# Kernel optimization log

Hardware: AMD Instinct MI355X
Metric: run time of the kernel (lower is better)

## Reference

```python
import jax, jax.numpy as jnp
import numpy as np

L, H, HD, D, FF, V, S_LEN = 12, 12, 64, 768, 3072, 50257, 1024
NEG = jnp.finfo(jnp.float32).min


def _ln(x, g, b, eps=1e-5):
    mu = x.mean(-1, keepdims=True)
    var = ((x - mu) ** 2).mean(-1, keepdims=True)
    return (x - mu) * jax.lax.rsqrt(var + eps) * g + b


def setup_inputs() -> dict:
    key = jax.random.key(0)
    ks = jax.random.split(key, 14)
    n = lambda k, shp, s=0.02: jax.random.normal(k, shp, jnp.float32) * s
    return {
        "input_ids": jax.random.randint(ks[0], (1, S_LEN), 0, V, dtype=jnp.int32),
        "attention_mask": jnp.ones((1, S_LEN), jnp.int32),
        "wte": n(ks[1], (V, D)),
        "wpe": n(ks[2], (S_LEN, D)),
        "ln1_g": 1.0 + n(ks[3], (L, D), 0.01),
        "ln1_b": n(ks[4], (L, D), 0.01),
        "W_qkv": n(ks[5], (L, D, 3 * D)),
        "b_qkv": n(ks[6], (L, 3 * D)),
        "W_o": n(ks[7], (L, D, D)),
        "b_o": n(ks[8], (L, D)),
        "ln2_g": 1.0 + n(ks[9], (L, D), 0.01),
        "ln2_b": n(ks[10], (L, D), 0.01),
        "W_fc": n(ks[11], (L, D, FF)),
        "b_fc": n(ks[12], (L, FF)),
        "W_proj": n(ks[13], (L, FF, D)),
        "b_proj": jnp.zeros((L, D), jnp.float32),
        "S": 20, "Sa1": 21, "S2": 600,
    }


def reference(input_ids, attention_mask, wte, wpe, ln1_g, ln1_b, W_qkv, b_qkv,
              W_o, b_o, ln2_g, ln2_b, W_fc, b_fc, W_proj, b_proj, S, Sa1, S2):
    T = input_ids.shape[-1]
    h0 = wte[input_ids[0]] + wpe[:T]                      # [T, D]
    causal = jnp.tril(jnp.ones((T, T), bool))
    add_mask = (1.0 - attention_mask[0].astype(jnp.float32)) * NEG  # [T]
    scale = 1.0 / np.sqrt(HD).astype(np.float32)

    def step(h, p):
        (l1g, l1b, Wqkv, bqkv, Wo, bo, l2g, l2b, Wfc, bfc, Wp, bp) = p
        xl = _ln(h, l1g, l1b)                             # pre-block LN, [T, D]
        # ---- standard GPT-2 block forward (advances hidden state) ----
        qkv = xl @ Wqkv + bqkv
        q, k, v = jnp.split(qkv, 3, axis=-1)
        q = q.reshape(T, H, HD).transpose(1, 0, 2)        # [H, T, HD]
        k = k.reshape(T, H, HD).transpose(1, 0, 2)
        v = v.reshape(T, H, HD).transpose(1, 0, 2)
        sc = jnp.einsum('hqd,hkd->hqk', q, k) * scale
        sc = jnp.where(causal, sc, NEG) + add_mask
        ctx = jnp.einsum('hqk,hkd->hqd', jax.nn.softmax(sc, axis=-1), v)
        attn_out = ctx.transpose(1, 0, 2).reshape(T, D) @ Wo + bo
        h2 = h + attn_out
        h_new = h2 + (jax.nn.gelu(_ln(h2, l2g, l2b) @ Wfc + bfc,
                                  approximate=True) @ Wp + bp)
        # ---- manual QK circuit decomposition (pre-block hidden state) ----
        Wq, Wk, _ = jnp.split(Wqkv, 3, axis=1)            # [D, D] each
        bq, bk, _ = jnp.split(bqkv, 3, axis=0)            # [D] each
        Wmhq = Wq.reshape(D, H, HD).transpose(1, 0, 2)    # [H, D, HD]
        Wmhk = Wk.reshape(D, H, HD).transpose(1, 0, 2)
        bqh = bq.reshape(H, HD)                           # [H, HD]
        bkh = bk.reshape(H, HD)
        qc = jnp.einsum('td,hdk->htk', xl, Wmhq)          # x W_q per head
        kc = jnp.einsum('td,hdk->htk', xl, Wmhk)          # x W_k per head
        term1 = jnp.einsum('hqk,htk->hqt', qc, kc)                 # x Wq Wk^T x^T
        term2 = jnp.einsum('hk,htk->ht', bqh, kc)[:, None, :]      # bq Wk^T x^T
        term3 = jnp.einsum('hqk,hk->hq', qc, bkh)[:, :, None]      # x Wq bk^T
        term4 = jnp.einsum('hk,hk->h', bqh, bkh)[:, None, None]    # bq bk^T
        scores = (term1 + term2 + term3 + term4) * scale
        aw = jax.nn.softmax(jnp.where(causal, scores, NEG), axis=-1)  # [H, T, T]
        dup = aw[:, S2, S]
        ind = aw[:, S2, Sa1]
        prev = aw[:, -1, S2]
        return h_new, (dup, ind, prev, prev)

    params = (ln1_g, ln1_b, W_qkv, b_qkv, W_o, b_o,
              ln2_g, ln2_b, W_fc, b_fc, W_proj, b_proj)
    _, (dup, ind, prev, name) = jax.lax.scan(step, h0, params)
    return dup, ind, prev, name   # each [L, H] = [12, 12]
```

## Files before the change

kernel.cpp:

```cpp
#include <hip/hip_runtime.h>
#include <hip/hip_bf16.h>
#include <math.h>

namespace {

constexpr int T = 1024;
constexpr int D = 768;
constexpr int FF = 3072;
constexpr int H = 12;
constexpr int HD = 64;
constexpr int L = 12;
constexpr float SCALE = 0.125f;

typedef __attribute__((ext_vector_type(8))) short short8;
typedef __attribute__((ext_vector_type(4))) float floatx4;

__device__ inline unsigned short f2bf(float f) {
    __hip_bfloat16 h = __float2bfloat16(f);
    return *reinterpret_cast<unsigned short*>(&h);
}
__device__ inline float bf2f(unsigned short u) {
    union { unsigned int i; float f; } c;
    c.i = (unsigned int)u << 16;
    return c.f;
}
__device__ inline void gld16(const void* g, void* l) {
    __builtin_amdgcn_global_load_lds(
        (const __attribute__((address_space(1))) void*)g,
        (__attribute__((address_space(3))) void*)l, 16, 0, 0);
}

__global__ void embed_kernel(const int* __restrict__ ids,
                             const float* __restrict__ wte,
                             const float* __restrict__ wpe,
                             float* __restrict__ h) {
    int i = blockIdx.x * blockDim.x + threadIdx.x;
    if (i >= T * D) return;
    int t = i / D, d = i % D;
    h[i] = wte[(long)ids[t] * D + d] + wpe[i];
}

__global__ __launch_bounds__(256)
void ln_kernel(const float* __restrict__ x, const float* __restrict__ g,
               const float* __restrict__ b, unsigned short* __restrict__ out) {
    int row = blockIdx.x, tid = threadIdx.x;
    const float* xr = x + (long)row * D;
    float v0 = xr[tid], v1 = xr[tid + 256], v2 = xr[tid + 512];
    __shared__ float red[4];
    __shared__ float share;
    float s = v0 + v1 + v2;
#pragma unroll
    for (int o = 32; o; o >>= 1) s += __shfl_down(s, o, 64);
    if ((tid & 63) == 0) red[tid >> 6] = s;
    __syncthreads();
    if (tid == 0) share = (red[0] + red[1] + red[2] + red[3]) * (1.0f / D);
    __syncthreads();
    float mu = share;
    float d0 = v0 - mu, d1 = v1 - mu, d2 = v2 - mu;
    float q = d0 * d0 + d1 * d1 + d2 * d2;
#pragma unroll
    for (int o = 32; o; o >>= 1) q += __shfl_down(q, o, 64);
    __syncthreads();
    if ((tid & 63) == 0) red[tid >> 6] = q;
    __syncthreads();
    if (tid == 0) share = rsqrtf((red[0] + red[1] + red[2] + red[3]) * (1.0f / D) + 1e-5f);
    __syncthreads();
    float rs = share;
    unsigned short* orow = out + (long)row * D;
    orow[tid]       = f2bf(d0 * rs * g[tid]       + b[tid]);
    orow[tid + 256] = f2bf(d1 * rs * g[tid + 256] + b[tid + 256]);
    orow[tid + 512] = f2bf(d2 * rs * g[tid + 512] + b[tid + 512]);
}

__global__ __launch_bounds__(256)
void wconvert_b(const float* __restrict__ W, unsigned short* __restrict__ WT,
                int K, int N) {
    const int zl = blockIdx.z;
    W  += (long)zl * K * N;
    WT += (long)zl * N * K;
    __shared__ float t[32][33];
    const int n0 = blockIdx.x * 32, k0 = blockIdx.y * 32;
    const int tx = threadIdx.x, ty = threadIdx.y;
#pragma unroll
    for (int i = 0; i < 4; i++)
        t[ty * 4 + i][tx] = W[(long)(k0 + ty * 4 + i) * N + n0 + tx];
    __syncthreads();
#pragma unroll
    for (int i = 0; i < 4; i++)
        WT[(long)(n0 + ty * 4 + i) * K + k0 + tx] = f2bf(t[tx][ty * 4 + i]);
}

#define GEMM_CORE(KLEN)                                                                 \
    floatx4 acc[2][4] = {};                                                             \
    gld16(ApA, &As[0][ablk][0][0]);                                                     \
    gld16(ApB, &As[0][ablk + 4][0][0]);                                                 \
    gld16(Bp,  &Bs[0][ablk][0][0]);                                                     \
    __syncthreads();                                                                    \
    const int nsteps = (KLEN) >> 5;                                                     \
    for (int s = 0; s < nsteps; s++) {                                                  \
        const int buf = s & 1;                                                          \
        const int nb = buf ^ 1;                                                         \
        if (s + 1 < nsteps) {                                                           \
            gld16(ApA + (s + 1) * 32, &As[nb][ablk][0][0]);                             \
            gld16(ApB + (s + 1) * 32, &As[nb][ablk + 4][0][0]);                         \
            gld16(Bp  + (s + 1) * 32, &Bs[nb][ablk][0][0]);                             \
        }                                                                               \
        short8 af[2], bfr[4];                                                           \
        _Pragma("unroll")                                                               \
        for (int mi = 0; mi < 2; mi++)                                                  \
            af[mi] = *(const short8*)&As[buf][w * 2 + mi][lane][0];                     \
        _Pragma("unroll")                                                               \
        for (int ni = 0; ni < 4; ni++)                                                  \
            bfr[ni] = *(const short8*)&Bs[buf][ni][lane][0];                            \
        _Pragma("unroll")                                                               \
        for (int mi = 0; mi < 2; mi++)                                                  \
            _Pragma("unroll")                                                           \
            for (int ni = 0; ni < 4; ni++)                                              \
                acc[mi][ni] = __builtin_amdgcn_mfma_f32_16x16x32_bf16(                  \
                    af[mi], bfr[ni], acc[mi][ni], 0, 0, 0);                             \
        __syncthreads();                                                                \
    }

#define GEMM_PRELUDE(KOFF)                                                              \
    const int tid = threadIdx.x;                                                        \
    const int w = tid >> 6, lane = tid & 63;                                            \
    const int ablk = tid >> 6;                                                          \
    const int sl = tid & 63;                                                            \
    const int row0 = blockIdx.y * 128, col0 = blockIdx.x * 64;                          \
    __shared__ unsigned short As[2][8][64][8];                                          \
    __shared__ unsigned short Bs[2][4][64][8];                                          \
    const unsigned short* ApA = A + (long)(row0 + ablk * 16 + (sl & 15)) * K + (KOFF) + (sl >> 4) * 8; \
    const unsigned short* ApB = ApA + 64L * K;                                          \
    const unsigned short* Bp  = BT + (long)(col0 + ablk * 16 + (sl & 15)) * K + (KOFF) + (sl >> 4) * 8;

__global__ __launch_bounds__(256)
void gemm_fused(const unsigned short* __restrict__ A, const unsigned short* __restrict__ BT,
                const float* __restrict__ bias, unsigned short* __restrict__ Cb,
                int N, int K, int flags) {
    GEMM_PRELUDE(0)
    GEMM_CORE(K)
#pragma unroll
    for (int mi = 0; mi < 2; mi++) {
        int rg = row0 + (w * 2 + mi) * 16 + (lane >> 4) * 4;
#pragma unroll
        for (int ni = 0; ni < 4; ni++) {
            int cg = col0 + ni * 16 + (lane & 15);
            float bv = (flags & 1) ? bias[cg] : 0.f;
            float bscale = ((flags & 16) && cg < D) ? SCALE : 1.0f;
#pragma unroll
            for (int r = 0; r < 4; r++) {
                float v = acc[mi][ni][r] + bv;
                if (flags & 4) {
                    float zz = 0.7978845608028654f * (v + 0.044715f * v * v * v);
                    v = v / (1.0f + __expf(-2.0f * zz));
                }
                Cb[(long)(rg + r) * N + cg] = f2bf(v * bscale);
            }
        }
    }
}

__global__ __launch_bounds__(256)
void gemm_bf16(const unsigned short* __restrict__ A, const unsigned short* __restrict__ BT,
               float* __restrict__ part, int N, int K, int splitK) {
    const int z = blockIdx.z;
    const int Kc = K / splitK;
    GEMM_PRELUDE(z * Kc)
    GEMM_CORE(Kc)
    float* dst = part + (long)z * T * N;
#pragma unroll
    for (int mi = 0; mi < 2; mi++) {
        int rg = row0 + (w * 2 + mi) * 16 + (lane >> 4) * 4;
#pragma unroll
        for (int ni = 0; ni < 4; ni++) {
            int cg = col0 + ni * 16 + (lane & 15);
#pragma unroll
            for (int r = 0; r < 4; r++)
                dst[(long)(rg + r) * N + cg] = acc[mi][ni][r];
        }
    }
}

__global__ __launch_bounds__(256)
void reduce_ln(const float* __restrict__ part, const float* __restrict__ bias,
               const float* __restrict__ resid,
               const float* __restrict__ g, const float* __restrict__ b,
               float* __restrict__ Cres, unsigned short* __restrict__ Cln,
               int splitK) {
    const int row = blockIdx.x, tid = threadIdx.x;
    const int c0 = tid, c1 = tid + 256, c2 = tid + 512;
    const long rb = (long)row * D;
    float v0 = bias[c0] + resid[rb + c0];
    float v1 = bias[c1] + resid[rb + c1];
    float v2 = bias[c2] + resid[rb + c2];
    for (int z = 0; z < splitK; z++) {
        const float* p = part + (long)z * T * D + rb;
        v0 += p[c0]; v1 += p[c1]; v2 += p[c2];
    }
    float* crow = Cres + rb;
    crow[c0] = v0; crow[c1] = v1; crow[c2] = v2;
    __shared__ float red[4];
    __shared__ float share;
    float s = v0 + v1 + v2;
#pragma unroll
    for (int o = 32; o; o >>= 1) s += __shfl_down(s, o, 64);
    if ((tid & 63) == 0) red[tid >> 6] = s;
    __syncthreads();
    if (tid == 0) share = (red[0] + red[1] + red[2] + red[3]) * (1.0f / D);
    __syncthreads();
    float mu = share;
    float d0 = v0 - mu, d1 = v1 - mu, d2 = v2 - mu;
    float q = d0 * d0 + d1 * d1 + d2 * d2;
#pragma unroll
    for (int o = 32; o; o >>= 1) q += __shfl_down(q, o, 64);
    __syncthreads();
    if ((tid & 63) == 0) red[tid >> 6] = q;
    __syncthreads();
    if (tid == 0) share = rsqrtf((red[0] + red[1] + red[2] + red[3]) * (1.0f / D) + 1e-5f);
    __syncthreads();
    float rs = share;
    unsigned short* orow = Cln + rb;
    orow[c0] = f2bf(d0 * rs * g[c0] + b[c0]);
    orow[c1] = f2bf(d1 * rs * g[c1] + b[c1]);
    orow[c2] = f2bf(d2 * rs * g[c2] + b[c2]);
}

__device__ void probe_body(const unsigned short* __restrict__ qkvb,
                           const int* __restrict__ Sp, const int* __restrict__ Sa1p,
                           const int* __restrict__ S2p,
                           float* __restrict__ out, int layer, int which, int h) {
    const int s = *Sp, sa1 = *Sa1p, s2 = *S2p;
    const int row = which ? (T - 1) : s2;
    const int tid = threadIdx.x;
    __shared__ float qrow[64];
    __shared__ float prob[T];
    __shared__ float red[4];
    __shared__ float bshare;
    if (tid < 64) qrow[tid] = bf2f(qkvb[(long)row * (3 * D) + h * HD + tid]);
    __syncthreads();
    float mloc = -INFINITY;
    for (int j = tid; j <= row; j += 256) {
        const unsigned short* krow = qkvb + (long)j * (3 * D) + D + h * HD;
        float acc = 0;
#pragma unroll
        for (int d = 0; d < 64; d += 8) {
            short8 kv = *(const short8*)(krow + d);
#pragma unroll
            for (int e = 0; e < 8; e++)
                acc += qrow[d + e] * bf2f((unsigned short)kv[e]);
        }
        prob[j] = acc;
        mloc = fmaxf(mloc, acc);
    }
#pragma unroll
    for (int o = 32; o; o >>= 1) mloc = fmaxf(mloc, __shfl_down(mloc, o, 64));
    if ((tid & 63) == 0) red[tid >> 6] = mloc;
    __syncthreads();
    if (tid == 0) bshare = fmaxf(fmaxf(red[0], red[1]), fmaxf(red[2], red[3]));
    __syncthreads();
    float m = bshare;
    float ssum = 0;
    for (int j = tid; j <= row; j += 256) {
        float e = expf(prob[j] - m);
        prob[j] = e;
        ssum += e;
    }
#pragma unroll
    for (int o = 32; o; o >>= 1) ssum += __shfl_down(ssum, o, 64);
    __syncthreads();
    if ((tid & 63) == 0) red[tid >> 6] = ssum;
    __syncthreads();
    if (tid == 0) bshare = red[0] + red[1] + red[2] + red[3];
    __syncthreads();
    float inv = 1.0f / bshare;
    if (tid == 0) {
        if (which == 0) {
            out[0 * (L * H) + layer * H + h] = prob[s] * inv;
            out[1 * (L * H) + layer * H + h] = prob[sa1] * inv;
        } else {
            out[2 * (L * H) + layer * H + h] = prob[s2] * inv;
            out[3 * (L * H) + layer * H + h] = prob[s2] * inv;
        }
    }
}

__global__ __launch_bounds__(256)
void probe_kernel(const unsigned short* __restrict__ qkvb,
                  const int* __restrict__ Sp, const int* __restrict__ Sa1p,
                  const int* __restrict__ S2p,
                  float* __restrict__ out, int layer) {
    probe_body(qkvb, Sp, Sa1p, S2p, out, layer, blockIdx.x, blockIdx.y);
}

__global__ __launch_bounds__(256)
void flash_probe(const unsigned short* __restrict__ qkvb, unsigned short* __restrict__ ctxb,
                 const int* __restrict__ Sp, const int* __restrict__ Sa1p,
                 const int* __restrict__ S2p, float* __restrict__ out, int layer) {
    const int h = blockIdx.y;
    if (blockIdx.x >= T / 64) {
        probe_body(qkvb, Sp, Sa1p, S2p, out, layer, blockIdx.x - T / 64, h);
        return;
    }
    const int q0 = blockIdx.x * 64;
    const int tid = threadIdx.x;
    const int w = tid >> 6;
    const int l = tid & 63;
    const int lm = l & 15;
    const int g = l >> 4;

    __shared__ unsigned short Kl[64][72];
    __shared__ unsigned short Vt[64][80];
    __shared__ unsigned short Pl[4][16][72];

    short8 qf[2];
    {
        const unsigned short* qp = qkvb + (long)(q0 + w * 16 + lm) * (3 * D) + h * HD + g * 8;
        qf[0] = *(const short8*)(qp);
        qf[1] = *(const short8*)(qp + 32);
    }

    const int d8 = (tid & 7) * 8;
    const int kp = (tid >> 3) * 2;

    float m = -INFINITY, lsum = 0.f;
    floatx4 o[4] = {};
    const int qw = q0 + w * 16;
    const int nt = blockIdx.x + 1;

    for (int t = 0; t < nt; t++) {
        const int c0 = t * 64;
        __syncthreads();
        {
            const unsigned short* kr0 = qkvb + (long)(c0 + kp) * (3 * D) + D + h * HD + d8;
            const unsigned short* kr1 = kr0 + 3 * D;
            *(short8*)&Kl[kp][d8]     = *(const short8*)kr0;
            *(short8*)&Kl[kp + 1][d8] = *(const short8*)kr1;
            short8 va = *(const short8*)(kr0 + D);
            short8 vb = *(const short8*)(kr1 + D);
#pragma unroll
            for (int j = 0; j < 8; j++) {
                unsigned int pk = (unsigned)(unsigned short)va[j] |
                                  ((unsigned)(unsigned short)vb[j] << 16);
                *(unsigned int*)&Vt[d8 + j][kp] = pk;
            }
        }
        __syncthreads();

        if (c0 > qw + 15) continue;

        floatx4 st[4] = {};
#pragma unroll
        for (int ks = 0; ks < 2; ks++)
#pragma unroll
            for (int mt = 0; mt < 4; mt++) {
                short8 af = *(const short8*)&Kl[mt * 16 + lm][ks * 32 + g * 8];
                st[mt] = __builtin_amdgcn_mfma_f32_16x16x32_bf16(af, qf[ks], st[mt], 0, 0, 0);
            }

        const int qg = qw + lm;
        if (c0 + 63 > qw) {
#pragma unroll
            for (int mt = 0; mt < 4; mt++)
#pragma unroll
                for (int r = 0; r < 4; r++)
                    if (c0 + mt * 16 + g * 4 + r > qg) st[mt][r] = -INFINITY;
        }
        float tmax = -INFINITY;
#pragma unroll
        for (int mt = 0; mt < 4; mt++)
#pragma unroll
            for (int r = 0; r < 4; r++) tmax = fmaxf(tmax, st[mt][r]);
        tmax = fmaxf(tmax, __shfl_xor(tmax, 16));
        tmax = fmaxf(tmax, __shfl_xor(tmax, 32));
        float mn = fmaxf(m, tmax);
        float alpha = __expf(m - mn);
        float psum = 0.f;
        unsigned short pb[16];
#pragma unroll
        for (int mt = 0; mt < 4; mt++)
#pragma unroll
            for (int r = 0; r < 4; r++) {
                float p = __expf(st[mt][r] - mn);
                psum += p;
                pb[mt * 4 + r] = f2bf(p);
            }
        lsum = lsum * alpha + psum;
        m = mn;
#pragma unroll
        for (int mt = 0; mt < 4; mt++) {
            unsigned int p0 = (unsigned)pb[mt * 4 + 0] | ((unsigned)pb[mt * 4 + 1] << 16);
            unsigned int p1 = (unsigned)pb[mt * 4 + 2] | ((unsigned)pb[mt * 4 + 3] << 16);
            *(unsigned int*)&Pl[w][lm][mt * 16 + g * 4]     = p0;
            *(unsigned int*)&Pl[w][lm][mt * 16 + g * 4 + 2] = p1;
        }
        float ar0 = __shfl(alpha, g * 4 + 0), ar1 = __shfl(alpha, g * 4 + 1);
        float ar2 = __shfl(alpha, g * 4 + 2), ar3 = __shfl(alpha, g * 4 + 3);
#pragma unroll
        for (int fd = 0; fd < 4; fd++) {
            o[fd][0] *= ar0; o[fd][1] *= ar1; o[fd][2] *= ar2; o[fd][3] *= ar3;
        }
#pragma unroll
        for (int ks = 0; ks < 2; ks++) {
            short8 pa = *(const short8*)&Pl[w][lm][ks * 32 + g * 8];
#pragma unroll
            for (int fd = 0; fd < 4; fd++) {
                short8 vb = *(const short8*)&Vt[fd * 16 + lm][ks * 32 + g * 8];
                o[fd] = __builtin_amdgcn_mfma_f32_16x16x32_bf16(pa, vb, o[fd], 0, 0, 0);
            }
        }
    }
    float l2 = lsum + __shfl_xor(lsum, 16);
    float l4 = l2 + __shfl_xor(l2, 32);
    float linv = 1.0f / l4;
    float lr0 = __shfl(linv, g * 4 + 0), lr1 = __shfl(linv, g * 4 + 1);
    float lr2 = __shfl(linv, g * 4 + 2), lr3 = __shfl(linv, g * 4 + 3);
#pragma unroll
    for (int fd = 0; fd < 4; fd++) {
        unsigned short* cp = ctxb + (long)(qw + g * 4) * D + h * HD + fd * 16 + lm;
        cp[0 * D] = f2bf(o[fd][0] * lr0);
        cp[1 * D] = f2bf(o[fd][1] * lr1);
        cp[2 * D] = f2bf(o[fd][2] * lr2);
        cp[3 * D] = f2bf(o[fd][3] * lr3);
    }
}

}

extern "C" void kernel_launch(void* const* d_in, const int* in_sizes, int n_in,
                              void* d_out, int out_size, void* d_ws, size_t ws_size,
                              hipStream_t stream) {
    const int*   ids    = (const int*)  d_in[0];
    const float* wte    = (const float*)d_in[2];
    const float* wpe    = (const float*)d_in[3];
    const float* ln1_g  = (const float*)d_in[4];
    const float* ln1_b  = (const float*)d_in[5];
    const float* W_qkv  = (const float*)d_in[6];
    const float* b_qkv  = (const float*)d_in[7];
    const float* W_o    = (const float*)d_in[8];
    const float* b_o    = (const float*)d_in[9];
    const float* ln2_g  = (const float*)d_in[10];
    const float* ln2_b  = (const float*)d_in[11];
    const float* W_fc   = (const float*)d_in[12];
    const float* b_fc   = (const float*)d_in[13];
    const float* W_proj = (const float*)d_in[14];
    const float* b_proj = (const float*)d_in[15];
    const int*   Sp     = (const int*)  d_in[16];
    const int*   Sa1p   = (const int*)  d_in[17];
    const int*   S2p    = (const int*)  d_in[18];
    float* out = (float*)d_out;

    float* ws   = (float*)d_ws;
    float* h    = ws;
    float* h2   = h   + (long)T * D;
    float* part = h2  + (long)T * D;
    unsigned short* xl   = (unsigned short*)(part + 4L * T * D);
    unsigned short* qkvb = xl   + (long)T * D;
    unsigned short* ctxb = qkvb + (long)T * 3 * D;
    unsigned short* fb   = ctxb + (long)T * D;
    unsigned short* wt_qkv  = fb      + (long)T * FF;
    unsigned short* wt_o    = wt_qkv  + (long)L * 3 * D * D;
    unsigned short* wt_fc   = wt_o    + (long)L * D * D;
    unsigned short* wt_proj = wt_fc   + (long)L * D * FF;

    embed_kernel<<<(T * D + 255) / 256, 256, 0, stream>>>(ids, wte, wpe, h);
    wconvert_b<<<dim3(3 * D / 32, D / 32, L), dim3(32, 8), 0, stream>>>(W_qkv, wt_qkv, D, 3 * D);
    wconvert_b<<<dim3(D / 32, D / 32, L), dim3(32, 8), 0, stream>>>(W_o, wt_o, D, D);
    wconvert_b<<<dim3(FF / 32, D / 32, L), dim3(32, 8), 0, stream>>>(W_fc, wt_fc, D, FF);
    wconvert_b<<<dim3(D / 32, FF / 32, L), dim3(32, 8), 0, stream>>>(W_proj, wt_proj, FF, D);
    ln_kernel<<<T, 256, 0, stream>>>(h, ln1_g, ln1_b, xl);

    for (int l = 0; l < L; l++) {
        gemm_fused<<<dim3(3 * D / 64, T / 128), 256, 0, stream>>>(
            xl, wt_qkv + (long)l * 3 * D * D, b_qkv + (long)l * 3 * D,
            qkvb, 3 * D, D, 1 | 16);

        if (l == L - 1) {
            probe_kernel<<<dim3(2, H), 256, 0, stream>>>(qkvb, Sp, Sa1p, S2p, out, l);
            break;
        }

        flash_probe<<<dim3(T / 64 + 2, H), 256, 0, stream>>>(
            qkvb, ctxb, Sp, Sa1p, S2p, out, l);
        gemm_bf16<<<dim3(D / 64, T / 128, 4), 256, 0, stream>>>(
            ctxb, wt_o + (long)l * D * D, part, D, D, 4);
        reduce_ln<<<T, 256, 0, stream>>>(
            part, b_o + (long)l * D, h, ln2_g + l * D, ln2_b + l * D, h2, xl, 4);
        gemm_fused<<<dim3(FF / 64, T / 128), 256, 0, stream>>>(
            xl, wt_fc + (long)l * D * FF, b_fc + (long)l * FF, fb, FF, D, 1 | 4);
        gemm_bf16<<<dim3(D / 64, T / 128, 4), 256, 0, stream>>>(
            fb, wt_proj + (long)l * D * FF, part, D, FF, 4);
        reduce_ln<<<T, 256, 0, stream>>>(
            part, b_proj + (long)l * D, h2, ln1_g + (l + 1) * D, ln1_b + (l + 1) * D, h, xl, 4);
    }
}
```

Measured before the change: 1.357 ms.

## Split attention key tiles across wave pairs with 32-query blocks and merge

The flash attention kernel now processes 32 queries per block instead of 64, with two waves sharing each 16-query group. Each wave in a pair handles half of every 64-key tile, and the two partial softmax states are merged through shared memory at the end. The goal is to double the number of blocks and remove idle waves on the causal diagonal, improving occupancy and load balance. In exchange, each block loads K/V tiles for fewer queries, adds a cross-wave reduction, and uses a finite mask value instead of -inf.

```diff
diff --git a/kernel.cpp b/kernel.cpp
--- a/kernel.cpp
+++ b/kernel.cpp
@@ -11,6 +11,7 @@
 constexpr int HD = 64;
 constexpr int L = 12;
 constexpr float SCALE = 0.125f;
+constexpr float MNEG = -1.0e30f;
 
 typedef __attribute__((ext_vector_type(8))) short short8;
 typedef __attribute__((ext_vector_type(4))) float floatx4;
@@ -297,13 +298,15 @@
                  const int* __restrict__ Sp, const int* __restrict__ Sa1p,
                  const int* __restrict__ S2p, float* __restrict__ out, int layer) {
     const int h = blockIdx.y;
-    if (blockIdx.x >= T / 64) {
-        probe_body(qkvb, Sp, Sa1p, S2p, out, layer, blockIdx.x - T / 64, h);
+    if (blockIdx.x >= T / 32) {
+        probe_body(qkvb, Sp, Sa1p, S2p, out, layer, blockIdx.x - T / 32, h);
         return;
     }
-    const int q0 = blockIdx.x * 64;
+    const int q0 = blockIdx.x * 32;
     const int tid = threadIdx.x;
     const int w = tid >> 6;
+    const int pair = w >> 1;
+    const int sub = w & 1;
     const int l = tid & 63;
     const int lm = l & 15;
     const int g = l >> 4;
@@ -312,9 +315,11 @@
     __shared__ unsigned short Vt[64][80];
     __shared__ unsigned short Pl[4][16][72];
 
+    const int qw = q0 + pair * 16;
+
     short8 qf[2];
     {
-        const unsigned short* qp = qkvb + (long)(q0 + w * 16 + lm) * (3 * D) + h * HD + g * 8;
+        const unsigned short* qp = qkvb + (long)(qw + lm) * (3 * D) + h * HD + g * 8;
         qf[0] = *(const short8*)(qp);
         qf[1] = *(const short8*)(qp + 32);
     }
@@ -322,10 +327,9 @@
     const int d8 = (tid & 7) * 8;
     const int kp = (tid >> 3) * 2;
 
-    float m = -INFINITY, lsum = 0.f;
+    float m = MNEG, lsum = 0.f;
     floatx4 o[4] = {};
-    const int qw = q0 + w * 16;
-    const int nt = blockIdx.x + 1;
+    const int nt = blockIdx.x / 2 + 1;
 
     for (int t = 0; t < nt; t++) {
         const int c0 = t * 64;
@@ -346,52 +350,48 @@
         }
         __syncthreads();
 
-        if (c0 > qw + 15) continue;
-
-        floatx4 st[4] = {};
+        floatx4 st[2] = {};
 #pragma unroll
         for (int ks = 0; ks < 2; ks++)
 #pragma unroll
-            for (int mt = 0; mt < 4; mt++) {
-                short8 af = *(const short8*)&Kl[mt * 16 + lm][ks * 32 + g * 8];
-                st[mt] = __builtin_amdgcn_mfma_f32_16x16x32_bf16(af, qf[ks], st[mt], 0, 0, 0);
+            for (int m2 = 0; m2 < 2; m2++) {
+                short8 af = *(const short8*)&Kl[(sub * 2 + m2) * 16 + lm][ks * 32 + g * 8];
+                st[m2] = __builtin_amdgcn_mfma_f32_16x16x32_bf16(af, qf[ks], st[m2], 0, 0, 0);
             }
 
         const int qg = qw + lm;
-        if (c0 + 63 > qw) {
-#pragma unroll
-            for (int mt = 0; mt < 4; mt++)
+        const int cb = c0 + sub * 32;
+        if (cb + 31 > qw) {
+#pragma unroll
+            for (int m2 = 0; m2 < 2; m2++)
 #pragma unroll
                 for (int r = 0; r < 4; r++)
-                    if (c0 + mt * 16 + g * 4 + r > qg) st[mt][r] = -INFINITY;
-        }
-        float tmax = -INFINITY;
-#pragma unroll
-        for (int mt = 0; mt < 4; mt++)
-#pragma unroll
-            for (int r = 0; r < 4; r++) tmax = fmaxf(tmax, st[mt][r]);
+                    if (cb + m2 * 16 + g * 4 + r > qg) st[m2][r] = MNEG;
+        }
+        float tmax = fmaxf(fmaxf(fmaxf(st[0][0], st[0][1]), fmaxf(st[0][2], st[0][3])),
+                           fmaxf(fmaxf(st[1][0], st[1][1]), fmaxf(st[1][2], st[1][3])));
         tmax = fmaxf(tmax, __shfl_xor(tmax, 16));
         tmax = fmaxf(tmax, __shfl_xor(tmax, 32));
         float mn = fmaxf(m, tmax);
         float alpha = __expf(m - mn);
         float psum = 0.f;
-        unsigned short pb[16];
-#pragma unroll
-        for (int mt = 0; mt < 4; mt++)
+        unsigned short pb[8];
+#pragma unroll
+        for (int m2 = 0; m2 < 2; m2++)
 #pragma unroll
             for (int r = 0; r < 4; r++) {
-                float p = __expf(st[mt][r] - mn);
+                float p = __expf(st[m2][r] - mn);
                 psum += p;
-                pb[mt * 4 + r] = f2bf(p);
+                pb[m2 * 4 + r] = f2bf(p);
             }
         lsum = lsum * alpha + psum;
         m = mn;
 #pragma unroll
-        for (int mt = 0; mt < 4; mt++) {
-            unsigned int p0 = (unsigned)pb[mt * 4 + 0] | ((unsigned)pb[mt * 4 + 1] << 16);
-            unsigned int p1 = (unsigned)pb[mt * 4 + 2] | ((unsigned)pb[mt * 4 + 3] << 16);
-            *(unsigned int*)&Pl[w][lm][mt * 16 + g * 4]     = p0;
-            *(unsigned int*)&Pl[w][lm][mt * 16 + g * 4 + 2] = p1;
+        for (int m2 = 0; m2 < 2; m2++) {
+            unsigned int p0 = (unsigned)pb[m2 * 4 + 0] | ((unsigned)pb[m2 * 4 + 1] << 16);
+            unsigned int p1 = (unsigned)pb[m2 * 4 + 2] | ((unsigned)pb[m2 * 4 + 3] << 16);
+            *(unsigned int*)&Pl[w][lm][(sub * 2 + m2) * 16 + g * 4]     = p0;
+            *(unsigned int*)&Pl[w][lm][(sub * 2 + m2) * 16 + g * 4 + 2] = p1;
         }
         float ar0 = __shfl(alpha, g * 4 + 0), ar1 = __shfl(alpha, g * 4 + 1);
         float ar2 = __shfl(alpha, g * 4 + 2), ar3 = __shfl(alpha, g * 4 + 3);
@@ -399,28 +399,48 @@
         for (int fd = 0; fd < 4; fd++) {
             o[fd][0] *= ar0; o[fd][1] *= ar1; o[fd][2] *= ar2; o[fd][3] *= ar3;
         }
-#pragma unroll
-        for (int ks = 0; ks < 2; ks++) {
-            short8 pa = *(const short8*)&Pl[w][lm][ks * 32 + g * 8];
+        {
+            short8 pa = *(const short8*)&Pl[w][lm][sub * 32 + g * 8];
 #pragma unroll
             for (int fd = 0; fd < 4; fd++) {
-                short8 vb = *(const short8*)&Vt[fd * 16 + lm][ks * 32 + g * 8];
+                short8 vb = *(const short8*)&Vt[fd * 16 + lm][sub * 32 + g * 8];
                 o[fd] = __builtin_amdgcn_mfma_f32_16x16x32_bf16(pa, vb, o[fd], 0, 0, 0);
             }
         }
     }
     float l2 = lsum + __shfl_xor(lsum, 16);
     float l4 = l2 + __shfl_xor(l2, 32);
-    float linv = 1.0f / l4;
-    float lr0 = __shfl(linv, g * 4 + 0), lr1 = __shfl(linv, g * 4 + 1);
-    float lr2 = __shfl(linv, g * 4 + 2), lr3 = __shfl(linv, g * 4 + 3);
-#pragma unroll
-    for (int fd = 0; fd < 4; fd++) {
-        unsigned short* cp = ctxb + (long)(qw + g * 4) * D + h * HD + fd * 16 + lm;
-        cp[0 * D] = f2bf(o[fd][0] * lr0);
-        cp[1 * D] = f2bf(o[fd][1] * lr1);
-        cp[2 * D] = f2bf(o[fd][2] * lr2);
-        cp[3 * D] = f2bf(o[fd][3] * lr3);
+
+    float* Om = (float*)&Kl[0][0];
+    float2* Mlb = (float2*)((char*)Om + 2 * 16 * 68 * 4);
+    __syncthreads();
+    if (sub == 1) {
+        if (g == 0) Mlb[pair * 16 + lm] = make_float2(m, l4);
+#pragma unroll
+        for (int fd = 0; fd < 4; fd++)
+#pragma unroll
+            for (int r = 0; r < 4; r++)
+                Om[(pair * 16 + g * 4 + r) * 68 + fd * 16 + lm] = o[fd][r];
+    }
+    __syncthreads();
+    if (sub == 0) {
+        float2 oth = Mlb[pair * 16 + lm];
+        float M = fmaxf(m, oth.x);
+        float e0 = __expf(m - M), e1 = __expf(oth.x - M);
+        float inv = 1.0f / (l4 * e0 + oth.y * e1);
+        float a0 = e0 * inv, a1 = e1 * inv;
+#pragma unroll
+        for (int fd = 0; fd < 4; fd++) {
+            unsigned short* cp = ctxb + (long)(qw + g * 4) * D + h * HD + fd * 16 + lm;
+#pragma unroll
+            for (int r = 0; r < 4; r++) {
+                float w0r = __shfl(a0, g * 4 + r);
+                float w1r = __shfl(a1, g * 4 + r);
+                float val = o[fd][r] * w0r +
+                            Om[(pair * 16 + g * 4 + r) * 68 + fd * 16 + lm] * w1r;
+                cp[(long)r * D] = f2bf(val);
+            }
+        }
     }
 }
 
@@ -479,7 +499,7 @@
             break;
         }
 
-        flash_probe<<<dim3(T / 64 + 2, H), 256, 0, stream>>>(
+        flash_probe<<<dim3(T / 32 + 2, H), 256, 0, stream>>>(
             qkvb, ctxb, Sp, Sa1p, S2p, out, l);
         gemm_bf16<<<dim3(D / 64, T / 128, 4), 256, 0, stream>>>(
             ctxb, wt_o + (long)l * D * D, part, D, D, 4);
```

Result: no change. 1.338 ms (-1.4%).
